# Optimization experiments

Hardware: AMD Instinct MI355X
Metric: run time of the kernel (lower is better)

## Reference

```python
import jax, jax.numpy as jnp
import numpy as np

N = 100000
E = 1000000
F_IN = 128
H = 64
C = 40


def _glorot(key, shape):
    fan_in, fan_out = shape[1], shape[0]
    lim = float(np.sqrt(6.0 / (fan_in + fan_out)))
    return jax.random.uniform(key, shape, jnp.float32, -lim, lim)


def setup_inputs() -> dict:
    key = jax.random.key(0)
    ks = jax.random.split(key, 8)
    x = jax.random.normal(ks[0], (N, F_IN), jnp.float32)
    edge_index = jax.random.randint(ks[1], (2, E), 0, N, jnp.int64)
    params = {
        # conv1: lin(F_IN->H), outer1(H->H), outer2(H->H)
        "w1_lin": _glorot(ks[2], (H, F_IN)), "b1_lin": jnp.zeros((H,), jnp.float32),
        "w1_o1": _glorot(ks[3], (H, H)), "b1_o1": jnp.zeros((H,), jnp.float32),
        "w1_o2": _glorot(ks[4], (H, H)), "b1_o2": jnp.zeros((H,), jnp.float32),
        # conv2: lin(H->C), outer1(C->C), outer2(C->C)
        "w2_lin": _glorot(ks[5], (C, H)), "b2_lin": jnp.zeros((C,), jnp.float32),
        "w2_o1": _glorot(ks[6], (C, C)), "b2_o1": jnp.zeros((C,), jnp.float32),
        "w2_o2": _glorot(ks[7], (C, C)), "b2_o2": jnp.zeros((C,), jnp.float32),
    }
    return {"x": x, "edge_index": edge_index, **params}


def gcn_conv(x, src, dst, w_lin, b_lin, w_o1, b_o1, w_o2, b_o2):
    # x: [N, Fin] -> lin -> [N, Fout]
    h = x @ w_lin.T + b_lin
    # propagate: gather h[src] ([E, Fout]) and scatter-add into dst;
    # self-loops (i -> i) are equivalent to adding h itself.
    agg = jax.ops.segment_sum(h[src], dst, num_segments=h.shape[0]) + h
    out = jax.nn.relu(agg)
    out = jax.nn.relu(out @ w_o1.T + b_o1)
    return out @ w_o2.T + b_o2


def reference(x, edge_index, w1_lin, b1_lin, w1_o1, b1_o1, w1_o2, b1_o2,
              w2_lin, b2_lin, w2_o1, b2_o1, w2_o2, b2_o2):
    src, dst = edge_index[0], edge_index[1]
    h = gcn_conv(x, src, dst, w1_lin, b1_lin, w1_o1, b1_o1, w1_o2, b1_o2)
    h = jax.nn.relu(h)
    # dropout is identity in eval mode (training=False)
    return gcn_conv(h, src, dst, w2_lin, b2_lin, w2_o1, b2_o1, w2_o2, b2_o2)
```

## Files before the change

kernel.cpp:

```cpp
#include <hip/hip_runtime.h>

static constexpr int FIN = 128;
static constexpr int HD  = 64;
static constexpr int CD  = 40;

typedef __attribute__((ext_vector_type(8))) short short8;
typedef __attribute__((ext_vector_type(4))) float f32x4;

__device__ __forceinline__ unsigned short f2b(float f)
{
    union { float f; unsigned u; } x; x.f = f;
    unsigned u = x.u;
    return (unsigned short)((u + 0x7FFF + ((u >> 16) & 1)) >> 16);
}
__device__ __forceinline__ float b2f(unsigned short b)
{
    union { unsigned u; float f; } x; x.u = ((unsigned)b) << 16;
    return x.f;
}

static constexpr int NBMAX = 512;
static constexpr int ACH   = 4096;

__global__ __launch_bounds__(256)
void prep_kernel(const float* __restrict__ w1_lin, const float* __restrict__ w1_o1,
                 const float* __restrict__ w1_o2, const float* __restrict__ w2_lin,
                 const float* __restrict__ w2_o1, const float* __restrict__ w2_o2,
                 unsigned short* __restrict__ wb, int* __restrict__ bucketCount)
{
    int i = blockIdx.x * 256 + threadIdx.x;
    if (i < NBMAX) bucketCount[i] = 0;
    if (i >= 25600) return;
    const float* src; int Kin, Kp, Oin, off;
    if (i < 8192)       { src = w1_lin; Kin = 128; Kp = 128; Oin = 64; off = 0; }
    else if (i < 12288) { src = w1_o1;  Kin = 64;  Kp = 64;  Oin = 64; off = 8192; }
    else if (i < 16384) { src = w1_o2;  Kin = 64;  Kp = 64;  Oin = 64; off = 12288; }
    else if (i < 19456) { src = w2_lin; Kin = 64;  Kp = 64;  Oin = 40; off = 16384; }
    else if (i < 22528) { src = w2_o1;  Kin = 40;  Kp = 64;  Oin = 40; off = 19456; }
    else                { src = w2_o2;  Kin = 40;  Kp = 64;  Oin = 40; off = 22528; }
    int j = i - off;
    int o = j / Kp, k = j - o * Kp;
    float v = (o < Oin && k < Kin) ? src[o * Kin + k] : 0.f;
    wb[i] = f2b(v);
}

template<int NKT, int NOT>
__device__ __forceinline__ void mfma_tile(const short8* a, const unsigned short* __restrict__ Wbf,
                                          int l16, int quad, f32x4* acc)
{
    constexpr int KP = NKT * 32;
#pragma unroll
    for (int ot = 0; ot < NOT; ++ot) {
        acc[ot] = (f32x4){0.f, 0.f, 0.f, 0.f};
        const unsigned short* Wrow = Wbf + (size_t)(ot * 16 + l16) * KP + quad * 8;
#pragma unroll
        for (int kt = 0; kt < NKT; ++kt) {
            short8 b = *reinterpret_cast<const short8*>(Wrow + kt * 32);
            acc[ot] = __builtin_amdgcn_mfma_f32_16x16x32_bf16(a[kt], b, acc[ot], 0, 0, 0);
        }
    }
}

__device__ __forceinline__ short8 relu_bf16x8(short8 v)
{
#pragma unroll
    for (int j = 0; j < 8; ++j) {
        unsigned short u = (unsigned short)v[j];
        if (u & 0x8000) v[j] = 0;
    }
    return v;
}

__global__ __launch_bounds__(256)
void mv1_bhist_kernel(const float* __restrict__ x, const unsigned short* __restrict__ wb1_lin,
                      const float* __restrict__ b1_lin, unsigned short* __restrict__ h,
                      int n, int tgrid,
                      const int* __restrict__ dst, int* __restrict__ bucketCount, int e, int nb)
{
    __shared__ int cnt[NBMAX];
    if (blockIdx.x >= tgrid) {
        const int bb = blockIdx.x - tgrid;
        const int t = threadIdx.x;
        for (int j = t; j < nb; j += 256) cnt[j] = 0;
        __syncthreads();
        const int i0 = bb * ACH;
        const int i1 = min(e, i0 + ACH);
        for (int i = i0 + t; i < i1; i += 256)
            atomicAdd(&cnt[dst[i] >> 8], 1);
        __syncthreads();
        for (int j = t; j < nb; j += 256)
            if (cnt[j]) atomicAdd(&bucketCount[j], cnt[j]);
        return;
    }
    const int t = threadIdx.x, wave = t >> 6, lane = t & 63;
    const int quad = lane >> 4, l16 = lane & 15;
    const int n0 = blockIdx.x * 64, m0 = wave * 16;
    int row = n0 + m0 + l16; if (row >= n) row = n - 1;

    short8 a[4];
#pragma unroll
    for (int kt = 0; kt < 4; ++kt) {
        const float* p = x + (size_t)row * FIN + kt * 32 + quad * 8;
        float4 f0 = *reinterpret_cast<const float4*>(p);
        float4 f1 = *reinterpret_cast<const float4*>(p + 4);
        short8 v;
        v[0] = (short)f2b(f0.x); v[1] = (short)f2b(f0.y);
        v[2] = (short)f2b(f0.z); v[3] = (short)f2b(f0.w);
        v[4] = (short)f2b(f1.x); v[5] = (short)f2b(f1.y);
        v[6] = (short)f2b(f1.z); v[7] = (short)f2b(f1.w);
        a[kt] = v;
    }
    f32x4 acc[4];
    mfma_tile<4, 4>(a, wb1_lin, l16, quad, acc);
#pragma unroll
    for (int ot = 0; ot < 4; ++ot) {
        int o = ot * 16 + l16;
        float bv = b1_lin[o];
#pragma unroll
        for (int r = 0; r < 4; ++r) {
            int node = n0 + m0 + quad * 4 + r;
            if (node < n) h[(size_t)node * HD + o] = f2b(acc[ot][r] + bv);
        }
    }
}

__global__ __launch_bounds__(256)
void chainB_kernel(const unsigned short* __restrict__ agg,
                   const unsigned short* __restrict__ wo1, const float* __restrict__ bo1,
                   const unsigned short* __restrict__ wo2, const float* __restrict__ bo2,
                   const unsigned short* __restrict__ wlin, const float* __restrict__ blin,
                   unsigned short* __restrict__ out, int n)
{
    constexpr int KS = 72;
    __shared__ unsigned short lds[64 * KS];
    const int t = threadIdx.x, wave = t >> 6, lane = t & 63;
    const int quad = lane >> 4, l16 = lane & 15;
    const int n0 = blockIdx.x * 64, m0 = wave * 16;
    int row = n0 + m0 + l16; if (row >= n) row = n - 1;

    short8 a[2];
#pragma unroll
    for (int kt = 0; kt < 2; ++kt) {
        short8 v = *reinterpret_cast<const short8*>(agg + (size_t)row * HD + kt * 32 + quad * 8);
        a[kt] = relu_bf16x8(v);
    }

    f32x4 acc[4];
    mfma_tile<2, 4>(a, wo1, l16, quad, acc);
#pragma unroll
    for (int ot = 0; ot < 4; ++ot) {
        int o = ot * 16 + l16;
        float bv = bo1[o];
#pragma unroll
        for (int r = 0; r < 4; ++r) {
            float v = fmaxf(acc[ot][r] + bv, 0.f);
            lds[(m0 + quad * 4 + r) * KS + o] = f2b(v);
        }
    }
#pragma unroll
    for (int kt = 0; kt < 2; ++kt)
        a[kt] = *reinterpret_cast<const short8*>(&lds[(m0 + l16) * KS + kt * 32 + quad * 8]);

    mfma_tile<2, 4>(a, wo2, l16, quad, acc);
#pragma unroll
    for (int ot = 0; ot < 4; ++ot) {
        int o = ot * 16 + l16;
        float bv = bo2[o];
#pragma unroll
        for (int r = 0; r < 4; ++r) {
            float v = fmaxf(acc[ot][r] + bv, 0.f);
            lds[(m0 + quad * 4 + r) * KS + o] = f2b(v);
        }
    }
#pragma unroll
    for (int kt = 0; kt < 2; ++kt)
        a[kt] = *reinterpret_cast<const short8*>(&lds[(m0 + l16) * KS + kt * 32 + quad * 8]);

    f32x4 acc3[3];
    mfma_tile<2, 3>(a, wlin, l16, quad, acc3);
#pragma unroll
    for (int ot = 0; ot < 3; ++ot) {
        int o = ot * 16 + l16;
        if (o < CD) {
            float bv = blin[o];
#pragma unroll
            for (int r = 0; r < 4; ++r) {
                int node = n0 + m0 + quad * 4 + r;
                if (node < n) out[(size_t)node * CD + o] = f2b(acc3[ot][r] + bv);
            }
        }
    }
}

__global__ __launch_bounds__(256)
void chainC_kernel(const unsigned short* __restrict__ agg,
                   const unsigned short* __restrict__ wo1, const float* __restrict__ bo1,
                   const unsigned short* __restrict__ wo2, const float* __restrict__ bo2,
                   float* __restrict__ out, int n)
{
    constexpr int KS = 72;
    __shared__ unsigned short lds[64 * KS];
    const int t = threadIdx.x, wave = t >> 6, lane = t & 63;
    const int quad = lane >> 4, l16 = lane & 15;
    const int n0 = blockIdx.x * 64, m0 = wave * 16;

    for (int i = lane; i < 16 * 16; i += 64) {
        int rr = i >> 4, cc = i & 15;
        lds[(m0 + rr) * KS + 48 + cc] = 0;
    }

    int row = n0 + m0 + l16; if (row >= n) row = n - 1;
    short8 a[2];
    {
        short8 v = *reinterpret_cast<const short8*>(agg + (size_t)row * CD + quad * 8);
        a[0] = relu_bf16x8(v);
    }
    {
        short8 v = {0, 0, 0, 0, 0, 0, 0, 0};
        if (quad == 0) {
            v = *reinterpret_cast<const short8*>(agg + (size_t)row * CD + 32);
            v = relu_bf16x8(v);
        }
        a[1] = v;
    }

    f32x4 acc[3];
    mfma_tile<2, 3>(a, wo1, l16, quad, acc);
#pragma unroll
    for (int ot = 0; ot < 3; ++ot) {
        int o = ot * 16 + l16;
        float bv = (o < CD) ? bo1[o] : 0.f;
#pragma unroll
        for (int r = 0; r < 4; ++r) {
            float v = (o < CD) ? fmaxf(acc[ot][r] + bv, 0.f) : 0.f;
            lds[(m0 + quad * 4 + r) * KS + o] = f2b(v);
        }
    }
#pragma unroll
    for (int kt = 0; kt < 2; ++kt)
        a[kt] = *reinterpret_cast<const short8*>(&lds[(m0 + l16) * KS + kt * 32 + quad * 8]);

    mfma_tile<2, 3>(a, wo2, l16, quad, acc);
#pragma unroll
    for (int ot = 0; ot < 3; ++ot) {
        int o = ot * 16 + l16;
        if (o < CD) {
            float bv = bo2[o];
#pragma unroll
            for (int r = 0; r < 4; ++r) {
                int node = n0 + m0 + quad * 4 + r;
                if (node < n) out[(size_t)node * CD + o] = acc[ot][r] + bv;
            }
        }
    }
}

__global__ __launch_bounds__(256)
void bscan_kernel(const int* __restrict__ bucketCount, int* __restrict__ bucketOff,
                  int* __restrict__ bucketCursor, int nb)
{
    __shared__ int sA[NBMAX], sB[NBMAX];
    const int t = threadIdx.x;
#pragma unroll
    for (int s = t; s < NBMAX; s += 256) sA[s] = (s < nb) ? bucketCount[s] : 0;
    __syncthreads();
    int* pa = sA; int* pb = sB;
    for (int off = 1; off < NBMAX; off <<= 1) {
#pragma unroll
        for (int s = t; s < NBMAX; s += 256)
            pb[s] = pa[s] + ((s >= off) ? pa[s - off] : 0);
        __syncthreads();
        int* tmp = pa; pa = pb; pb = tmp;
    }
#pragma unroll
    for (int s = t; s <= nb && s < NBMAX; s += 256) {
        int v = (s == 0) ? 0 : pa[s - 1];
        bucketOff[s] = v;
        if (s < nb) bucketCursor[s] = v;
    }
}

__global__ __launch_bounds__(256)
void bpart_kernel(const int* __restrict__ src, const int* __restrict__ dst,
                  int* __restrict__ bucketCursor, uint2* __restrict__ pairs,
                  int e, int nb)
{
    __shared__ int cnt[NBMAX];
    __shared__ int base[NBMAX];
    const int t = threadIdx.x;
    for (int j = t; j < nb; j += 256) cnt[j] = 0;
    __syncthreads();
    const int i0 = blockIdx.x * ACH;
    const int i1 = min(e, i0 + ACH);
    for (int i = i0 + t; i < i1; i += 256)
        atomicAdd(&cnt[dst[i] >> 8], 1);
    __syncthreads();
    for (int j = t; j < nb; j += 256) {
        int c = cnt[j];
        base[j] = c ? atomicAdd(&bucketCursor[j], c) : 0;
        cnt[j] = 0;
    }
    __syncthreads();
    for (int i = i0 + t; i < i1; i += 256) {
        int d = dst[i];
        int bkt = d >> 8;
        int pos = base[bkt] + atomicAdd(&cnt[bkt], 1);
        pairs[pos] = make_uint2((unsigned)d, (unsigned)src[i]);
    }
}

__global__ __launch_bounds__(256)
void bbuild_kernel(const uint2* __restrict__ pairs, const int* __restrict__ bucketOff,
                   int* __restrict__ rowptr_end, int* __restrict__ deg_g,
                   int* __restrict__ eidx, int n)
{
    __shared__ int deg[256], sA[256], sB[256], cur[256];
    const int t = threadIdx.x;
    const int b = blockIdx.x;
    const int node0 = b << 8;
    const int e0 = bucketOff[b], e1 = bucketOff[b + 1];

    deg[t] = 0;
    __syncthreads();
    for (int i = e0 + t; i < e1; i += 256)
        atomicAdd(&deg[pairs[i].x & 255], 1);
    __syncthreads();
    sA[t] = deg[t];
    __syncthreads();
    int* pa = sA; int* pb = sB;
    for (int off = 1; off < 256; off <<= 1) {
        pb[t] = pa[t] + ((t >= off) ? pa[t - off] : 0);
        __syncthreads();
        int* tmp = pa; pa = pb; pb = tmp;
    }
    const int node = node0 + t;
    if (node < n) {
        rowptr_end[node] = e0 + pa[t];
        deg_g[node] = deg[t];
    }
    cur[t] = pa[t] - deg[t];
    __syncthreads();
    for (int i = e0 + t; i < e1; i += 256) {
        uint2 p = pairs[i];
        int pos = e0 + atomicAdd(&cur[p.x & 255], 1);
        eidx[pos] = (int)p.y;
    }
}

template<int D>
__global__ __launch_bounds__(256)
void gather_bf16_kernel(const int* __restrict__ rowptr_end, const int* __restrict__ deg,
                        const int* __restrict__ eidx, const unsigned short* __restrict__ h,
                        unsigned short* __restrict__ agg, int n)
{
    const int wave = threadIdx.x >> 6;
    const int lane = threadIdx.x & 63;
    const int grp  = lane >> 4;
    const int l16  = lane & 15;
    const int node = blockIdx.x * 16 + wave * 4 + grp;
    const int nodec = (node < n) ? node : (n - 1);
    constexpr int LPN = D / 4;
    const bool act = (l16 < LPN) && (node < n);
    const int c0 = l16 * 4;

    float a0 = 0.f, a1 = 0.f, a2 = 0.f, a3 = 0.f;
    if (act) {
        ushort4 v = *reinterpret_cast<const ushort4*>(h + (size_t)nodec * D + c0);
        a0 = b2f(v.x); a1 = b2f(v.y); a2 = b2f(v.z); a3 = b2f(v.w);
    }
    int end   = rowptr_end[nodec];
    int start = end - deg[nodec];
    if (node >= n) end = start;

    for (int base = start; base < end; base += 16) {
        int m = min(16, end - base);
        int sv = (l16 < m) ? eidx[base + l16] : 0;
        for (int j = 0; j < m; ++j) {
            int s = __shfl(sv, grp * 16 + j, 64);
            if (act) {
                ushort4 v = *reinterpret_cast<const ushort4*>(h + (size_t)s * D + c0);
                a0 += b2f(v.x); a1 += b2f(v.y); a2 += b2f(v.z); a3 += b2f(v.w);
            }
        }
    }
    if (act) {
        ushort4 o;
        o.x = f2b(a0); o.y = f2b(a1); o.z = f2b(a2); o.w = f2b(a3);
        *reinterpret_cast<ushort4*>(agg + (size_t)node * D + c0) = o;
    }
}

extern "C" void kernel_launch(void* const* d_in, const int* in_sizes, int n_in,
                              void* d_out, int out_size, void* d_ws, size_t ws_size,
                              hipStream_t stream)
{
    const float* x      = (const float*)d_in[0];
    const int*   ei     = (const int*)d_in[1];
    const float* w1_lin = (const float*)d_in[2];
    const float* b1_lin = (const float*)d_in[3];
    const float* w1_o1  = (const float*)d_in[4];
    const float* b1_o1  = (const float*)d_in[5];
    const float* w1_o2  = (const float*)d_in[6];
    const float* b1_o2  = (const float*)d_in[7];
    const float* w2_lin = (const float*)d_in[8];
    const float* b2_lin = (const float*)d_in[9];
    const float* w2_o1  = (const float*)d_in[10];
    const float* b2_o1  = (const float*)d_in[11];
    const float* w2_o2  = (const float*)d_in[12];
    const float* b2_o2  = (const float*)d_in[13];

    const int n = in_sizes[0] / FIN;
    const int e = in_sizes[1] / 2;
    const int* src = ei;
    const int* dst = ei + e;

    unsigned short* ws0 = (unsigned short*)d_ws;
    unsigned short* ws1 = ws0 + (size_t)n * HD;
    unsigned short* wb  = ws1 + (size_t)n * HD;
    unsigned short* wb1_lin = wb;
    unsigned short* wb1_o1  = wb1_lin + 64 * 128;
    unsigned short* wb1_o2  = wb1_o1  + 64 * 64;
    unsigned short* wb2_lin = wb1_o2  + 64 * 64;
    unsigned short* wb2_o1  = wb2_lin + 48 * 64;
    unsigned short* wb2_o2  = wb2_o1  + 48 * 64;
    uint2* pairs        = (uint2*)(wb2_o2 + 48 * 64);
    int*   bucketCount  = (int*)(pairs + e);
    int*   bucketOff    = bucketCount + NBMAX;
    int*   bucketCursor = bucketOff + NBMAX + 1;
    float* outp = (float*)d_out;

    int* eidx   = (int*)d_out;
    int* deg    = eidx + e;
    int* rowptr = deg + n;

    const int nb    = (n + 255) >> 8;
    const int agrid = (e + ACH - 1) / ACH;
    const int tgrid = (n + 63) / 64;
    const int ggrid = (n + 15) / 16;

    prep_kernel<<<(25600 + 255) / 256, 256, 0, stream>>>(
        w1_lin, w1_o1, w1_o2, w2_lin, w2_o1, w2_o2, wb, bucketCount);

    mv1_bhist_kernel<<<tgrid + agrid, 256, 0, stream>>>(
        x, wb1_lin, b1_lin, ws0, n, tgrid, dst, bucketCount, e, nb);

    bscan_kernel<<<1, 256, 0, stream>>>(bucketCount, bucketOff, bucketCursor, nb);
    bpart_kernel<<<agrid, 256, 0, stream>>>(src, dst, bucketCursor, pairs, e, nb);
    bbuild_kernel<<<nb, 256, 0, stream>>>(pairs, bucketOff, rowptr, deg, eidx, n);

    gather_bf16_kernel<HD><<<ggrid, 256, 0, stream>>>(rowptr, deg, eidx, ws0, ws1, n);

    chainB_kernel<<<tgrid, 256, 0, stream>>>(
        ws1, wb1_o1, b1_o1, wb1_o2, b1_o2, wb2_lin, b2_lin, ws0, n);

    gather_bf16_kernel<CD><<<ggrid, 256, 0, stream>>>(rowptr, deg, eidx, ws0, ws1, n);

    chainC_kernel<<<tgrid, 256, 0, stream>>>(
        ws1, wb2_o1, b2_o1, wb2_o2, b2_o2, outp, n);
}
```

Measured before the change: 275.2 us.

## Gather with one wave per node over 8 parallel edges and pad layer-2 rows

Rewrites the neighbor aggregation so each wave handles one node. Eight lane groups each load a different edge's 16-byte row chunk, two edges in flight per iteration, and the partial sums are reduced with cross-lane shuffles. The old kernel put 16 lanes on a node and walked its edges one after another with 8-byte loads. The layer-2 intermediate is padded from 40 to a 48-column stride, zero-filled, so rows can be read as aligned 16-byte vectors. The aim is more memory-level parallelism and wider loads in the latency-bound gather, at the cost of idle lanes for low-degree nodes and a shuffle reduction per node.

```diff
diff --git a/kernel.cpp b/kernel.cpp
--- a/kernel.cpp
+++ b/kernel.cpp
@@ -3,6 +3,7 @@
 static constexpr int FIN = 128;
 static constexpr int HD  = 64;
 static constexpr int CD  = 40;
+static constexpr int S2  = 48;
 
 typedef __attribute__((ext_vector_type(8))) short short8;
 typedef __attribute__((ext_vector_type(4))) float f32x4;
@@ -181,12 +182,13 @@
 #pragma unroll
     for (int ot = 0; ot < 3; ++ot) {
         int o = ot * 16 + l16;
-        if (o < CD) {
-            float bv = blin[o];
-#pragma unroll
-            for (int r = 0; r < 4; ++r) {
-                int node = n0 + m0 + quad * 4 + r;
-                if (node < n) out[(size_t)node * CD + o] = f2b(acc3[ot][r] + bv);
+        float bv = (o < CD) ? blin[o] : 0.f;
+#pragma unroll
+        for (int r = 0; r < 4; ++r) {
+            int node = n0 + m0 + quad * 4 + r;
+            if (node < n) {
+                float v = (o < CD) ? (acc3[ot][r] + bv) : 0.f;
+                out[(size_t)node * S2 + o] = f2b(v);
             }
         }
     }
@@ -212,13 +214,13 @@
     int row = n0 + m0 + l16; if (row >= n) row = n - 1;
     short8 a[2];
     {
-        short8 v = *reinterpret_cast<const short8*>(agg + (size_t)row * CD + quad * 8);
+        short8 v = *reinterpret_cast<const short8*>(agg + (size_t)row * S2 + quad * 8);
         a[0] = relu_bf16x8(v);
     }
     {
         short8 v = {0, 0, 0, 0, 0, 0, 0, 0};
         if (quad == 0) {
-            v = *reinterpret_cast<const short8*>(agg + (size_t)row * CD + 32);
+            v = *reinterpret_cast<const short8*>(agg + (size_t)row * S2 + 32);
             v = relu_bf16x8(v);
         }
         a[1] = v;
@@ -347,46 +349,66 @@
     }
 }
 
-template<int D>
-__global__ __launch_bounds__(256)
-void gather_bf16_kernel(const int* __restrict__ rowptr_end, const int* __restrict__ deg,
-                        const int* __restrict__ eidx, const unsigned short* __restrict__ h,
-                        unsigned short* __restrict__ agg, int n)
-{
-    const int wave = threadIdx.x >> 6;
-    const int lane = threadIdx.x & 63;
-    const int grp  = lane >> 4;
-    const int l16  = lane & 15;
-    const int node = blockIdx.x * 16 + wave * 4 + grp;
-    const int nodec = (node < n) ? node : (n - 1);
-    constexpr int LPN = D / 4;
-    const bool act = (l16 < LPN) && (node < n);
-    const int c0 = l16 * 4;
-
-    float a0 = 0.f, a1 = 0.f, a2 = 0.f, a3 = 0.f;
-    if (act) {
-        ushort4 v = *reinterpret_cast<const ushort4*>(h + (size_t)nodec * D + c0);
-        a0 = b2f(v.x); a1 = b2f(v.y); a2 = b2f(v.z); a3 = b2f(v.w);
-    }
-    int end   = rowptr_end[nodec];
-    int start = end - deg[nodec];
-    if (node >= n) end = start;
+template<int STRIDE, int CHUNKS>
+__global__ __launch_bounds__(256)
+void gatherw_kernel(const int* __restrict__ rowptr_end, const int* __restrict__ deg_g,
+                    const int* __restrict__ eidx, const unsigned short* __restrict__ h,
+                    unsigned short* __restrict__ agg, int n)
+{
+    const int wave = threadIdx.x >> 6, lane = threadIdx.x & 63;
+    const int ec = lane >> 3;
+    const int ch = lane & 7;
+    const int node = blockIdx.x * 4 + wave;
+    if (node >= n) return;
+
+    const bool chact = (ch < CHUNKS);
+    float a[8] = {0.f, 0.f, 0.f, 0.f, 0.f, 0.f, 0.f, 0.f};
+
+    if (ec == 0 && chact) {
+        union { uint4 u; unsigned short s[8]; } v;
+        v.u = *reinterpret_cast<const uint4*>(h + (size_t)node * STRIDE + ch * 8);
+#pragma unroll
+        for (int j = 0; j < 8; ++j) a[j] = b2f(v.s[j]);
+    }
+
+    const int end   = rowptr_end[node];
+    const int start = end - deg_g[node];
 
     for (int base = start; base < end; base += 16) {
-        int m = min(16, end - base);
-        int sv = (l16 < m) ? eidx[base + l16] : 0;
-        for (int j = 0; j < m; ++j) {
-            int s = __shfl(sv, grp * 16 + j, 64);
-            if (act) {
-                ushort4 v = *reinterpret_cast<const ushort4*>(h + (size_t)s * D + c0);
-                a0 += b2f(v.x); a1 += b2f(v.y); a2 += b2f(v.z); a3 += b2f(v.w);
-            }
-        }
-    }
-    if (act) {
-        ushort4 o;
-        o.x = f2b(a0); o.y = f2b(a1); o.z = f2b(a2); o.w = f2b(a3);
-        *reinterpret_cast<ushort4*>(agg + (size_t)node * D + c0) = o;
+        const int i0 = base + ec, i1 = base + 8 + ec;
+        const bool v0 = (i0 < end) && chact;
+        const bool v1 = (i1 < end) && chact;
+        union { uint4 u; unsigned short s[8]; } u0, u1;
+        if (v0) {
+            int s = eidx[i0];
+            u0.u = *reinterpret_cast<const uint4*>(h + (size_t)s * STRIDE + ch * 8);
+        }
+        if (v1) {
+            int s = eidx[i1];
+            u1.u = *reinterpret_cast<const uint4*>(h + (size_t)s * STRIDE + ch * 8);
+        }
+        if (v0) {
+#pragma unroll
+            for (int j = 0; j < 8; ++j) a[j] += b2f(u0.s[j]);
+        }
+        if (v1) {
+#pragma unroll
+            for (int j = 0; j < 8; ++j) a[j] += b2f(u1.s[j]);
+        }
+    }
+
+#pragma unroll
+    for (int j = 0; j < 8; ++j) {
+        a[j] += __shfl_xor(a[j], 8, 64);
+        a[j] += __shfl_xor(a[j], 16, 64);
+        a[j] += __shfl_xor(a[j], 32, 64);
+    }
+
+    if (ec == 0 && chact) {
+        union { uint4 u; unsigned short s[8]; } o;
+#pragma unroll
+        for (int j = 0; j < 8; ++j) o.s[j] = f2b(a[j]);
+        *reinterpret_cast<uint4*>(agg + (size_t)node * STRIDE + ch * 8) = o.u;
     }
 }
 
@@ -436,7 +458,7 @@
     const int nb    = (n + 255) >> 8;
     const int agrid = (e + ACH - 1) / ACH;
     const int tgrid = (n + 63) / 64;
-    const int ggrid = (n + 15) / 16;
+    const int wgrid = (n + 3) / 4;
 
     prep_kernel<<<(25600 + 255) / 256, 256, 0, stream>>>(
         w1_lin, w1_o1, w1_o2, w2_lin, w2_o1, w2_o2, wb, bucketCount);
@@ -448,12 +470,12 @@
     bpart_kernel<<<agrid, 256, 0, stream>>>(src, dst, bucketCursor, pairs, e, nb);
     bbuild_kernel<<<nb, 256, 0, stream>>>(pairs, bucketOff, rowptr, deg, eidx, n);
 
-    gather_bf16_kernel<HD><<<ggrid, 256, 0, stream>>>(rowptr, deg, eidx, ws0, ws1, n);
+    gatherw_kernel<HD, 8><<<wgrid, 256, 0, stream>>>(rowptr, deg, eidx, ws0, ws1, n);
 
     chainB_kernel<<<tgrid, 256, 0, stream>>>(
         ws1, wb1_o1, b1_o1, wb1_o2, b1_o2, wb2_lin, b2_lin, ws0, n);
 
-    gather_bf16_kernel<CD><<<ggrid, 256, 0, stream>>>(rowptr, deg, eidx, ws0, ws1, n);
+    gatherw_kernel<S2, 6><<<wgrid, 256, 0, stream>>>(rowptr, deg, eidx, ws0, ws1, n);
 
     chainC_kernel<<<tgrid, 256, 0, stream>>>(
         ws1, wb2_o1, b2_o1, wb2_o2, b2_o2, outp, n);
```

Result: slower. 295.7 us (+7.4%).

## Fuse neighbor gather into MLP chain kernels with shared-memory slabs

Applied to the files above, without the earlier changes.

Merges each gather/aggregation kernel with the following MLP chain kernel. Neighbor sums are accumulated into a 16-node shared-memory slab and fed straight into the MFMA matmuls, so the intermediate aggregate never goes through global memory. Because the output buffer is overwritten, the CSR arrays are first copied into the pairs region by extra blocks in the first fused kernel. Layer-2 features are also padded to a 48-wide stride. In exchange, each block now handles 16 nodes instead of 64, so MFMA utilization per block drops and some waves sit idle.

```diff
diff --git a/kernel.cpp b/kernel.cpp
--- a/kernel.cpp
+++ b/kernel.cpp
@@ -3,6 +3,8 @@
 static constexpr int FIN = 128;
 static constexpr int HD  = 64;
 static constexpr int CD  = 40;
+static constexpr int S2  = 48;
+static constexpr int SLB = 72;
 
 typedef __attribute__((ext_vector_type(8))) short short8;
 typedef __attribute__((ext_vector_type(4))) float f32x4;
@@ -61,14 +63,19 @@
     }
 }
 
-__device__ __forceinline__ short8 relu_bf16x8(short8 v)
-{
-#pragma unroll
-    for (int j = 0; j < 8; ++j) {
-        unsigned short u = (unsigned short)v[j];
-        if (u & 0x8000) v[j] = 0;
-    }
-    return v;
+__device__ __forceinline__ f32x4 mv16(const unsigned short* slab,
+                                      const unsigned short* __restrict__ Wbf,
+                                      int o, int l16, int quad)
+{
+    short8 a0 = *reinterpret_cast<const short8*>(&slab[l16 * SLB + quad * 8]);
+    short8 a1 = *reinterpret_cast<const short8*>(&slab[l16 * SLB + 32 + quad * 8]);
+    const unsigned short* Wrow = Wbf + (size_t)o * 64 + quad * 8;
+    short8 b0 = *reinterpret_cast<const short8*>(Wrow);
+    short8 b1 = *reinterpret_cast<const short8*>(Wrow + 32);
+    f32x4 acc = (f32x4){0.f, 0.f, 0.f, 0.f};
+    acc = __builtin_amdgcn_mfma_f32_16x16x32_bf16(a0, b0, acc, 0, 0, 0);
+    acc = __builtin_amdgcn_mfma_f32_16x16x32_bf16(a1, b1, acc, 0, 0, 0);
+    return acc;
 }
 
 __global__ __launch_bounds__(256)
@@ -125,137 +132,6 @@
 }
 
 __global__ __launch_bounds__(256)
-void chainB_kernel(const unsigned short* __restrict__ agg,
-                   const unsigned short* __restrict__ wo1, const float* __restrict__ bo1,
-                   const unsigned short* __restrict__ wo2, const float* __restrict__ bo2,
-                   const unsigned short* __restrict__ wlin, const float* __restrict__ blin,
-                   unsigned short* __restrict__ out, int n)
-{
-    constexpr int KS = 72;
-    __shared__ unsigned short lds[64 * KS];
-    const int t = threadIdx.x, wave = t >> 6, lane = t & 63;
-    const int quad = lane >> 4, l16 = lane & 15;
-    const int n0 = blockIdx.x * 64, m0 = wave * 16;
-    int row = n0 + m0 + l16; if (row >= n) row = n - 1;
-
-    short8 a[2];
-#pragma unroll
-    for (int kt = 0; kt < 2; ++kt) {
-        short8 v = *reinterpret_cast<const short8*>(agg + (size_t)row * HD + kt * 32 + quad * 8);
-        a[kt] = relu_bf16x8(v);
-    }
-
-    f32x4 acc[4];
-    mfma_tile<2, 4>(a, wo1, l16, quad, acc);
-#pragma unroll
-    for (int ot = 0; ot < 4; ++ot) {
-        int o = ot * 16 + l16;
-        float bv = bo1[o];
-#pragma unroll
-        for (int r = 0; r < 4; ++r) {
-            float v = fmaxf(acc[ot][r] + bv, 0.f);
-            lds[(m0 + quad * 4 + r) * KS + o] = f2b(v);
-        }
-    }
-#pragma unroll
-    for (int kt = 0; kt < 2; ++kt)
-        a[kt] = *reinterpret_cast<const short8*>(&lds[(m0 + l16) * KS + kt * 32 + quad * 8]);
-
-    mfma_tile<2, 4>(a, wo2, l16, quad, acc);
-#pragma unroll
-    for (int ot = 0; ot < 4; ++ot) {
-        int o = ot * 16 + l16;
-        float bv = bo2[o];
-#pragma unroll
-        for (int r = 0; r < 4; ++r) {
-            float v = fmaxf(acc[ot][r] + bv, 0.f);
-            lds[(m0 + quad * 4 + r) * KS + o] = f2b(v);
-        }
-    }
-#pragma unroll
-    for (int kt = 0; kt < 2; ++kt)
-        a[kt] = *reinterpret_cast<const short8*>(&lds[(m0 + l16) * KS + kt * 32 + quad * 8]);
-
-    f32x4 acc3[3];
-    mfma_tile<2, 3>(a, wlin, l16, quad, acc3);
-#pragma unroll
-    for (int ot = 0; ot < 3; ++ot) {
-        int o = ot * 16 + l16;
-        if (o < CD) {
-            float bv = blin[o];
-#pragma unroll
-            for (int r = 0; r < 4; ++r) {
-                int node = n0 + m0 + quad * 4 + r;
-                if (node < n) out[(size_t)node * CD + o] = f2b(acc3[ot][r] + bv);
-            }
-        }
-    }
-}
-
-__global__ __launch_bounds__(256)
-void chainC_kernel(const unsigned short* __restrict__ agg,
-                   const unsigned short* __restrict__ wo1, const float* __restrict__ bo1,
-                   const unsigned short* __restrict__ wo2, const float* __restrict__ bo2,
-                   float* __restrict__ out, int n)
-{
-    constexpr int KS = 72;
-    __shared__ unsigned short lds[64 * KS];
-    const int t = threadIdx.x, wave = t >> 6, lane = t & 63;
-    const int quad = lane >> 4, l16 = lane & 15;
-    const int n0 = blockIdx.x * 64, m0 = wave * 16;
-
-    for (int i = lane; i < 16 * 16; i += 64) {
-        int rr = i >> 4, cc = i & 15;
-        lds[(m0 + rr) * KS + 48 + cc] = 0;
-    }
-
-    int row = n0 + m0 + l16; if (row >= n) row = n - 1;
-    short8 a[2];
-    {
-        short8 v = *reinterpret_cast<const short8*>(agg + (size_t)row * CD + quad * 8);
-        a[0] = relu_bf16x8(v);
-    }
-    {
-        short8 v = {0, 0, 0, 0, 0, 0, 0, 0};
-        if (quad == 0) {
-            v = *reinterpret_cast<const short8*>(agg + (size_t)row * CD + 32);
-            v = relu_bf16x8(v);
-        }
-        a[1] = v;
-    }
-
-    f32x4 acc[3];
-    mfma_tile<2, 3>(a, wo1, l16, quad, acc);
-#pragma unroll
-    for (int ot = 0; ot < 3; ++ot) {
-        int o = ot * 16 + l16;
-        float bv = (o < CD) ? bo1[o] : 0.f;
-#pragma unroll
-        for (int r = 0; r < 4; ++r) {
-            float v = (o < CD) ? fmaxf(acc[ot][r] + bv, 0.f) : 0.f;
-            lds[(m0 + quad * 4 + r) * KS + o] = f2b(v);
-        }
-    }
-#pragma unroll
-    for (int kt = 0; kt < 2; ++kt)
-        a[kt] = *reinterpret_cast<const short8*>(&lds[(m0 + l16) * KS + kt * 32 + quad * 8]);
-
-    mfma_tile<2, 3>(a, wo2, l16, quad, acc);
-#pragma unroll
-    for (int ot = 0; ot < 3; ++ot) {
-        int o = ot * 16 + l16;
-        if (o < CD) {
-            float bv = bo2[o];
-#pragma unroll
-            for (int r = 0; r < 4; ++r) {
-                int node = n0 + m0 + quad * 4 + r;
-                if (node < n) out[(size_t)node * CD + o] = acc[ot][r] + bv;
-            }
-        }
-    }
-}
-
-__global__ __launch_bounds__(256)
 void bscan_kernel(const int* __restrict__ bucketCount, int* __restrict__ bucketOff,
                   int* __restrict__ bucketCursor, int nb)
 {
@@ -347,29 +223,25 @@
     }
 }
 
-template<int D>
-__global__ __launch_bounds__(256)
-void gather_bf16_kernel(const int* __restrict__ rowptr_end, const int* __restrict__ deg,
-                        const int* __restrict__ eidx, const unsigned short* __restrict__ h,
-                        unsigned short* __restrict__ agg, int n)
-{
-    const int wave = threadIdx.x >> 6;
-    const int lane = threadIdx.x & 63;
-    const int grp  = lane >> 4;
-    const int l16  = lane & 15;
-    const int node = blockIdx.x * 16 + wave * 4 + grp;
+template<int STRIDE, int LPN>
+__device__ __forceinline__ void gather_relu_slab(
+    const int* __restrict__ rowptr_end, const int* __restrict__ deg_g,
+    const int* __restrict__ eidx, const unsigned short* __restrict__ h,
+    unsigned short* slabA, int node0, int n, int wave, int grp, int l16)
+{
+    const int r16 = wave * 4 + grp;
+    const int node = node0 + r16;
     const int nodec = (node < n) ? node : (n - 1);
-    constexpr int LPN = D / 4;
-    const bool act = (l16 < LPN) && (node < n);
+    const bool act = (l16 < LPN);
     const int c0 = l16 * 4;
 
     float a0 = 0.f, a1 = 0.f, a2 = 0.f, a3 = 0.f;
     if (act) {
-        ushort4 v = *reinterpret_cast<const ushort4*>(h + (size_t)nodec * D + c0);
+        ushort4 v = *reinterpret_cast<const ushort4*>(h + (size_t)nodec * STRIDE + c0);
         a0 = b2f(v.x); a1 = b2f(v.y); a2 = b2f(v.z); a3 = b2f(v.w);
     }
     int end   = rowptr_end[nodec];
-    int start = end - deg[nodec];
+    int start = end - deg_g[nodec];
     if (node >= n) end = start;
 
     for (int base = start; base < end; base += 16) {
@@ -378,15 +250,121 @@
         for (int j = 0; j < m; ++j) {
             int s = __shfl(sv, grp * 16 + j, 64);
             if (act) {
-                ushort4 v = *reinterpret_cast<const ushort4*>(h + (size_t)s * D + c0);
+                ushort4 v = *reinterpret_cast<const ushort4*>(h + (size_t)s * STRIDE + c0);
                 a0 += b2f(v.x); a1 += b2f(v.y); a2 += b2f(v.z); a3 += b2f(v.w);
             }
         }
     }
     if (act) {
         ushort4 o;
-        o.x = f2b(a0); o.y = f2b(a1); o.z = f2b(a2); o.w = f2b(a3);
-        *reinterpret_cast<ushort4*>(agg + (size_t)node * D + c0) = o;
+        o.x = f2b(fmaxf(a0, 0.f)); o.y = f2b(fmaxf(a1, 0.f));
+        o.z = f2b(fmaxf(a2, 0.f)); o.w = f2b(fmaxf(a3, 0.f));
+        *reinterpret_cast<ushort4*>(&slabA[r16 * SLB + c0]) = o;
+    }
+}
+
+__global__ __launch_bounds__(256)
+void gchainB_kernel(const int* __restrict__ rowptr_end, const int* __restrict__ deg_g,
+                    const int* __restrict__ eidx, const unsigned short* __restrict__ h,
+                    const unsigned short* __restrict__ wo1, const float* __restrict__ bo1,
+                    const unsigned short* __restrict__ wo2, const float* __restrict__ bo2,
+                    const unsigned short* __restrict__ wlin, const float* __restrict__ blin,
+                    unsigned short* __restrict__ out, int n, int ggrid,
+                    const int4* __restrict__ csr_src, int4* __restrict__ csr_dst, int c4)
+{
+    if (blockIdx.x >= ggrid) {
+        const int stride = (gridDim.x - ggrid) * 256;
+        for (int i = (blockIdx.x - ggrid) * 256 + threadIdx.x; i < c4; i += stride)
+            csr_dst[i] = csr_src[i];
+        return;
+    }
+
+    __shared__ unsigned short slabA[16 * SLB];
+    __shared__ unsigned short slabB[16 * SLB];
+    const int t = threadIdx.x, wave = t >> 6, lane = t & 63;
+    const int quad = lane >> 4, l16 = lane & 15;
+    const int node0 = blockIdx.x * 16;
+
+    gather_relu_slab<HD, 16>(rowptr_end, deg_g, eidx, h, slabA, node0, n, wave, quad, l16);
+    __syncthreads();
+
+    {
+        int o = wave * 16 + l16;
+        f32x4 acc = mv16(slabA, wo1, o, l16, quad);
+        float bv = bo1[o];
+#pragma unroll
+        for (int r = 0; r < 4; ++r)
+            slabB[(quad * 4 + r) * SLB + o] = f2b(fmaxf(acc[r] + bv, 0.f));
+    }
+    __syncthreads();
+    {
+        int o = wave * 16 + l16;
+        f32x4 acc = mv16(slabB, wo2, o, l16, quad);
+        float bv = bo2[o];
+#pragma unroll
+        for (int r = 0; r < 4; ++r)
+            slabA[(quad * 4 + r) * SLB + o] = f2b(fmaxf(acc[r] + bv, 0.f));
+    }
+    __syncthreads();
+    if (wave < 3) {
+        int o = wave * 16 + l16;
+        f32x4 acc = mv16(slabA, wlin, o, l16, quad);
+        float bv = (o < CD) ? blin[o] : 0.f;
+#pragma unroll
+        for (int r = 0; r < 4; ++r) {
+            int node = node0 + quad * 4 + r;
+            if (node < n) {
+                float v = (o < CD) ? (acc[r] + bv) : 0.f;
+                out[(size_t)node * S2 + o] = f2b(v);
+            }
+        }
+    }
+}
+
+__global__ __launch_bounds__(256)
+void gchainC_kernel(const int* __restrict__ rowptr_end, const int* __restrict__ deg_g,
+                    const int* __restrict__ eidx, const unsigned short* __restrict__ h2,
+                    const unsigned short* __restrict__ wo1, const float* __restrict__ bo1,
+                    const unsigned short* __restrict__ wo2, const float* __restrict__ bo2,
+                    float* __restrict__ out, int n)
+{
+    __shared__ unsigned short slabA[16 * SLB];
+    __shared__ unsigned short slabB[16 * SLB];
+    const int t = threadIdx.x, wave = t >> 6, lane = t & 63;
+    const int quad = lane >> 4, l16 = lane & 15;
+    const int node0 = blockIdx.x * 16;
+
+    for (int i = t; i < 16 * 16; i += 256) {
+        int rr = i >> 4, cc = i & 15;
+        slabA[rr * SLB + 48 + cc] = 0;
+        slabB[rr * SLB + 48 + cc] = 0;
+    }
+
+    gather_relu_slab<S2, 12>(rowptr_end, deg_g, eidx, h2, slabA, node0, n, wave, quad, l16);
+    __syncthreads();
+
+    if (wave < 3) {
+        int o = wave * 16 + l16;
+        f32x4 acc = mv16(slabA, wo1, o, l16, quad);
+        float bv = (o < CD) ? bo1[o] : 0.f;
+#pragma unroll
+        for (int r = 0; r < 4; ++r) {
+            float v = (o < CD) ? fmaxf(acc[r] + bv, 0.f) : 0.f;
+            slabB[(quad * 4 + r) * SLB + o] = f2b(v);
+        }
+    }
+    __syncthreads();
+    if (wave < 3) {
+        int o = wave * 16 + l16;
+        f32x4 acc = mv16(slabB, wo2, o, l16, quad);
+        if (o < CD) {
+            float bv = bo2[o];
+#pragma unroll
+            for (int r = 0; r < 4; ++r) {
+                int node = node0 + quad * 4 + r;
+                if (node < n) out[(size_t)node * CD + o] = acc[r] + bv;
+            }
+        }
     }
 }
 
@@ -415,8 +393,8 @@
     const int* dst = ei + e;
 
     unsigned short* ws0 = (unsigned short*)d_ws;
-    unsigned short* ws1 = ws0 + (size_t)n * HD;
-    unsigned short* wb  = ws1 + (size_t)n * HD;
+    unsigned short* ws2 = ws0 + (size_t)n * HD;
+    unsigned short* wb  = ws2 + (size_t)n * S2;
     unsigned short* wb1_lin = wb;
     unsigned short* wb1_o1  = wb1_lin + 64 * 128;
     unsigned short* wb1_o2  = wb1_o1  + 64 * 64;
@@ -432,11 +410,16 @@
     int* eidx   = (int*)d_out;
     int* deg    = eidx + e;
     int* rowptr = deg + n;
+    int* ceidx   = (int*)pairs;
+    int* cdeg    = ceidx + e;
+    int* crowptr = cdeg + n;
 
     const int nb    = (n + 255) >> 8;
     const int agrid = (e + ACH - 1) / ACH;
     const int tgrid = (n + 63) / 64;
     const int ggrid = (n + 15) / 16;
+    const int cgrid = 150;
+    const int c4    = (e + 2 * n) / 4;
 
     prep_kernel<<<(25600 + 255) / 256, 256, 0, stream>>>(
         w1_lin, w1_o1, w1_o2, w2_lin, w2_o1, w2_o2, wb, bucketCount);
@@ -448,13 +431,10 @@
     bpart_kernel<<<agrid, 256, 0, stream>>>(src, dst, bucketCursor, pairs, e, nb);
     bbuild_kernel<<<nb, 256, 0, stream>>>(pairs, bucketOff, rowptr, deg, eidx, n);
 
-    gather_bf16_kernel<HD><<<ggrid, 256, 0, stream>>>(rowptr, deg, eidx, ws0, ws1, n);
-
-    chainB_kernel<<<tgrid, 256, 0, stream>>>(
-        ws1, wb1_o1, b1_o1, wb1_o2, b1_o2, wb2_lin, b2_lin, ws0, n);
-
-    gather_bf16_kernel<CD><<<ggrid, 256, 0, stream>>>(rowptr, deg, eidx, ws0, ws1, n);
-
-    chainC_kernel<<<tgrid, 256, 0, stream>>>(
-        ws1, wb2_o1, b2_o1, wb2_o2, b2_o2, outp, n);
-}
+    gchainB_kernel<<<ggrid + cgrid, 256, 0, stream>>>(
+        rowptr, deg, eidx, ws0, wb1_o1, b1_o1, wb1_o2, b1_o2, wb2_lin, b2_lin,
+        ws2, n, ggrid, (const int4*)eidx, (int4*)ceidx, c4);
+
+    gchainC_kernel<<<ggrid, 256, 0, stream>>>(
+        crowptr, cdeg, ceidx, ws2, wb2_o1, b2_o1, wb2_o2, b2_o2, outp, n);
+}
```

Result: faster. 257.1 us (-6.6%).
